# Performance work log

Measured on AMD Instinct MI355X. Metric: run time of the kernel, lower is better.

The kernel has to match this reference:

```python
import jax, jax.numpy as jnp
import numpy as np


def _interpn_linear(vol, loc):
    """Trilinear interpolation matching voxelmorph/neuron interpn.
    vol: [X, Y, Z, C]; loc: [X, Y, Z, 3] absolute sample coordinates.
    """
    spatial = vol.shape[:-1]
    ndims = len(spatial)
    max_f = jnp.asarray([d - 1 for d in spatial], dtype=loc.dtype)
    max_i = jnp.asarray([d - 1 for d in spatial], dtype=jnp.int32)

    loc = jnp.clip(loc, 0.0, max_f)          # clipped_loc
    loc0 = jnp.floor(loc)
    loc0i = jnp.clip(loc0.astype(jnp.int32), 0, max_i)
    loc1i = jnp.clip(loc0i + 1, 0, max_i)

    # voxelmorph weights: corner-0 weight = loc1 - clipped_loc, corner-1 = 1 - that
    w_lo = loc1i.astype(loc.dtype) - loc      # weight for taking loc0
    w_hi = 1.0 - w_lo                          # weight for taking loc1

    out = jnp.zeros(vol.shape, vol.dtype)
    for c in range(2 ** ndims):
        bits = [(c >> d) & 1 for d in range(ndims)]
        idx = tuple(jnp.where(bits[d], loc1i[..., d], loc0i[..., d]) if False else (loc1i[..., d] if bits[d] else loc0i[..., d]) for d in range(ndims))
        w = jnp.ones(loc.shape[:-1], loc.dtype)
        for d in range(ndims):
            w = w * (w_hi[..., d] if bits[d] else w_lo[..., d])
        out = out + vol[idx] * w[..., None]
    return out


def setup_inputs() -> dict:
    key = jax.random.key(0)
    k1, k2 = jax.random.split(key)
    vol = jax.random.normal(k1, (2, 160, 160, 160, 1), dtype=jnp.float32)
    flow = jax.random.normal(k2, (2, 160, 160, 160, 3), dtype=jnp.float32)
    return {"vol": vol, "flow": flow}


def reference(vol, flow):
    # dense displacement field: absolute location = identity grid + flow
    spatial = vol.shape[1:-1]
    grid = jnp.stack(
        jnp.meshgrid(*[jnp.arange(d, dtype=flow.dtype) for d in spatial], indexing="ij"),
        axis=-1,
    )  # [X,Y,Z,3]
    loc = grid[None] + flow  # [B,X,Y,Z,3]
    return jax.vmap(_interpn_linear)(vol, loc)
```

## Files before the change

### kernel.cpp

```cpp
#include <hip/hip_runtime.h>


typedef float f32x4 __attribute__((ext_vector_type(4)));
typedef float f32x2 __attribute__((ext_vector_type(2), aligned(4)));

#define DIM 160
#define DD  (DIM * DIM)
#define DDD (DIM * DIM * DIM)
#define BATCH 2
#define TOTAL (BATCH * DDD)
#define BLK 256
#define NBLK (TOTAL / BLK)
#define NXCD 8
#define CHUNK (NBLK / NXCD)

__global__ __launch_bounds__(256) void st_warp_kernel(
    const float* __restrict__ vol,
    const float* __restrict__ flow,
    float* __restrict__ out)
{
    __shared__ float sflow[BLK * 3];

    int tid = threadIdx.x;
    int bid = blockIdx.x;
    int swz  = (bid & 7) * CHUNK + (bid >> 3);
    int base = swz * BLK;

    const f32x4* fsrc = (const f32x4*)(flow + (size_t)base * 3);
    if (tid < 192) {
        f32x4 v = __builtin_nontemporal_load(&fsrc[tid]);
        ((f32x4*)sflow)[tid] = v;
    }
    __syncthreads();

    int idx = base + tid;

    int b   = idx / DDD;
    int rem = idx - b * DDD;
    int x   = rem / DD;
    int r2  = rem - x * DD;
    int y   = r2 / DIM;
    int z   = r2 - y * DIM;

    float fx = sflow[tid * 3 + 0];
    float fy = sflow[tid * 3 + 1];
    float fz = sflow[tid * 3 + 2];

    const float maxf = (float)(DIM - 1);

    float lx = fminf(fmaxf((float)x + fx, 0.0f), maxf);
    float ly = fminf(fmaxf((float)y + fy, 0.0f), maxf);
    float lz = fminf(fmaxf((float)z + fz, 0.0f), maxf);

    int x0 = (int)floorf(lx);
    int y0 = (int)floorf(ly);
    int z0 = (int)floorf(lz);
    x0 = min(max(x0, 0), DIM - 1);
    y0 = min(max(y0, 0), DIM - 1);
    z0 = min(max(z0, 0), DIM - 1);

    int x1 = min(x0 + 1, DIM - 1);
    int y1 = min(y0 + 1, DIM - 1);
    int z1 = min(z0 + 1, DIM - 1);

    float wx0 = (float)x1 - lx;  float wx1 = 1.0f - wx0;
    float wy0 = (float)y1 - ly;  float wy1 = 1.0f - wy0;
    float wz0 = (float)z1 - lz;  float wz1 = 1.0f - wz0;

    const float* vb = vol + (size_t)b * DDD;

    int bx0 = x0 * DD, bx1 = x1 * DD;
    int by0 = y0 * DIM, by1 = y1 * DIM;

    int zb = min(z0, DIM - 2);
    f32x2 p00 = *(const f32x2*)(vb + bx0 + by0 + zb);
    f32x2 p10 = *(const f32x2*)(vb + bx1 + by0 + zb);
    f32x2 p01 = *(const f32x2*)(vb + bx0 + by1 + zb);
    f32x2 p11 = *(const f32x2*)(vb + bx1 + by1 + zb);

    float v000 = p00.x, v001 = p00.y;
    float v100 = p10.x, v101 = p10.y;
    float v010 = p01.x, v011 = p01.y;
    float v110 = p11.x, v111 = p11.y;

    float acc;
    acc  = v000 * (wx0 * wy0 * wz0);
    acc += v100 * (wx1 * wy0 * wz0);
    acc += v010 * (wx0 * wy1 * wz0);
    acc += v110 * (wx1 * wy1 * wz0);
    acc += v001 * (wx0 * wy0 * wz1);
    acc += v101 * (wx1 * wy0 * wz1);
    acc += v011 * (wx0 * wy1 * wz1);
    acc += v111 * (wx1 * wy1 * wz1);

    __builtin_nontemporal_store(acc, &out[idx]);
}

extern "C" void kernel_launch(void* const* d_in, const int* in_sizes, int n_in,
                              void* d_out, int out_size, void* d_ws, size_t ws_size,
                              hipStream_t stream)
{
    const float* vol  = (const float*)d_in[0];
    const float* flow = (const float*)d_in[1];
    float* out = (float*)d_out;

    st_warp_kernel<<<NBLK, BLK, 0, stream>>>(vol, flow, out);
}
```

Measured before the change: 212.5 us.

## Tile blocks as 4x4x16 bricks for 3D gather locality

Each block now covers a 4x4x16 brick of output voxels instead of 256 contiguous z-voxels (about 1.6 rows). Flow is staged per row into padded shared memory, and the results are transposed through shared memory so the global stores stay contiguous along z. The within-wave thread mapping also changes: each 64-lane wavefront now covers a 4x4x4 cube rather than 64 consecutive z-voxels. The goal is better L2/cache reuse of the trilinear gathers, since neighbouring x/y voxels touch overlapping vol lines. The cost is an extra barrier, shared-memory traffic, and flow loads split into 64-byte row segments that are less coalesced.

```diff
diff --git a/kernel.cpp b/kernel.cpp
--- a/kernel.cpp
+++ b/kernel.cpp
@@ -8,53 +8,68 @@
 #define DD  (DIM * DIM)
 #define DDD (DIM * DIM * DIM)
 #define BATCH 2
-#define TOTAL (BATCH * DDD)
 #define BLK 256
-#define NBLK (TOTAL / BLK)
-#define NXCD 8
-#define CHUNK (NBLK / NXCD)
+#define NBX 40
+#define NBY 40
+#define NBZ 10
+#define NBLK (BATCH * NBX * NBY * NBZ)
+#define CHUNK (NBLK / 8)
+
+#define FROW 52
 
 __global__ __launch_bounds__(256) void st_warp_kernel(
     const float* __restrict__ vol,
     const float* __restrict__ flow,
     float* __restrict__ out)
 {
-    __shared__ float sflow[BLK * 3];
+    __shared__ float sflow[16 * FROW];
+    __shared__ float sout[BLK];
 
     int tid = threadIdx.x;
     int bid = blockIdx.x;
-    int swz  = (bid & 7) * CHUNK + (bid >> 3);
-    int base = swz * BLK;
+    int swz = (bid & 7) * CHUNK + (bid >> 3);
 
-    const f32x4* fsrc = (const f32x4*)(flow + (size_t)base * 3);
+    int bb = swz / (NBX * NBY * NBZ);
+    int r  = swz - bb * (NBX * NBY * NBZ);
+    int xb = r / (NBY * NBZ);
+    int r2 = r - xb * (NBY * NBZ);
+    int yb = r2 / NBZ;
+    int zb = r2 - yb * NBZ;
+
+    int x0b = xb * 4, y0b = yb * 4, z0b = zb * 16;
+
     if (tid < 192) {
-        f32x4 v = __builtin_nontemporal_load(&fsrc[tid]);
-        ((f32x4*)sflow)[tid] = v;
+        int rr = tid / 12;
+        int q  = tid - rr * 12;
+        int xr = x0b + (rr >> 2);
+        int yr = y0b + (rr & 3);
+        const f32x4* src = (const f32x4*)(flow +
+            ((size_t)((bb * DIM + xr) * DIM + yr) * DIM + z0b) * 3);
+        f32x4 v = __builtin_nontemporal_load(&src[q]);
+        *(f32x4*)&sflow[rr * FROW + q * 4] = v;
     }
     __syncthreads();
 
-    int idx = base + tid;
+    int lx  = (tid >> 4) & 3;
+    int ly  = (tid >> 2) & 3;
+    int lz  = ((tid >> 6) << 2) | (tid & 3);
+    int row = (lx << 2) | ly;
 
-    int b   = idx / DDD;
-    int rem = idx - b * DDD;
-    int x   = rem / DD;
-    int r2  = rem - x * DD;
-    int y   = r2 / DIM;
-    int z   = r2 - y * DIM;
+    float fx = sflow[row * FROW + lz * 3 + 0];
+    float fy = sflow[row * FROW + lz * 3 + 1];
+    float fz = sflow[row * FROW + lz * 3 + 2];
 
-    float fx = sflow[tid * 3 + 0];
-    float fy = sflow[tid * 3 + 1];
-    float fz = sflow[tid * 3 + 2];
+    int x = x0b + lx, y = y0b + ly, z = z0b + lz;
 
     const float maxf = (float)(DIM - 1);
 
-    float lx = fminf(fmaxf((float)x + fx, 0.0f), maxf);
-    float ly = fminf(fmaxf((float)y + fy, 0.0f), maxf);
-    float lz = fminf(fmaxf((float)z + fz, 0.0f), maxf);
+    float lxf = fminf(fmaxf((float)x + fx, 0.0f), maxf);
+    float lyf = fminf(fmaxf((float)y + fy, 0.0f), maxf);
+    float lzf = fminf(fmaxf((float)z + fz, 0.0f), maxf);
 
-    int x0 = (int)floorf(lx);
-    int y0 = (int)floorf(ly);
-    int z0 = (int)floorf(lz);
+    int x0 = (int)floorf(lxf);
+    int y0 = (int)floorf(lyf);
+    int z0 = (int)floorf(lzf);
     x0 = min(max(x0, 0), DIM - 1);
     y0 = min(max(y0, 0), DIM - 1);
     z0 = min(max(z0, 0), DIM - 1);
@@ -63,37 +78,41 @@
     int y1 = min(y0 + 1, DIM - 1);
     int z1 = min(z0 + 1, DIM - 1);
 
-    float wx0 = (float)x1 - lx;  float wx1 = 1.0f - wx0;
-    float wy0 = (float)y1 - ly;  float wy1 = 1.0f - wy0;
-    float wz0 = (float)z1 - lz;  float wz1 = 1.0f - wz0;
+    float wx0 = (float)x1 - lxf;  float wx1 = 1.0f - wx0;
+    float wy0 = (float)y1 - lyf;  float wy1 = 1.0f - wy0;
+    float wz0 = (float)z1 - lzf;  float wz1 = 1.0f - wz0;
 
-    const float* vb = vol + (size_t)b * DDD;
-
+    const float* vb = vol + (size_t)bb * DDD;
     int bx0 = x0 * DD, bx1 = x1 * DD;
     int by0 = y0 * DIM, by1 = y1 * DIM;
 
-    int zb = min(z0, DIM - 2);
-    f32x2 p00 = *(const f32x2*)(vb + bx0 + by0 + zb);
-    f32x2 p10 = *(const f32x2*)(vb + bx1 + by0 + zb);
-    f32x2 p01 = *(const f32x2*)(vb + bx0 + by1 + zb);
-    f32x2 p11 = *(const f32x2*)(vb + bx1 + by1 + zb);
-
-    float v000 = p00.x, v001 = p00.y;
-    float v100 = p10.x, v101 = p10.y;
-    float v010 = p01.x, v011 = p01.y;
-    float v110 = p11.x, v111 = p11.y;
+    int zp = min(z0, DIM - 2);
+    f32x2 p00 = *(const f32x2*)(vb + bx0 + by0 + zp);
+    f32x2 p10 = *(const f32x2*)(vb + bx1 + by0 + zp);
+    f32x2 p01 = *(const f32x2*)(vb + bx0 + by1 + zp);
+    f32x2 p11 = *(const f32x2*)(vb + bx1 + by1 + zp);
 
     float acc;
-    acc  = v000 * (wx0 * wy0 * wz0);
-    acc += v100 * (wx1 * wy0 * wz0);
-    acc += v010 * (wx0 * wy1 * wz0);
-    acc += v110 * (wx1 * wy1 * wz0);
-    acc += v001 * (wx0 * wy0 * wz1);
-    acc += v101 * (wx1 * wy0 * wz1);
-    acc += v011 * (wx0 * wy1 * wz1);
-    acc += v111 * (wx1 * wy1 * wz1);
+    acc  = p00.x * (wx0 * wy0 * wz0);
+    acc += p10.x * (wx1 * wy0 * wz0);
+    acc += p01.x * (wx0 * wy1 * wz0);
+    acc += p11.x * (wx1 * wy1 * wz0);
+    acc += p00.y * (wx0 * wy0 * wz1);
+    acc += p10.y * (wx1 * wy0 * wz1);
+    acc += p01.y * (wx0 * wy1 * wz1);
+    acc += p11.y * (wx1 * wy1 * wz1);
 
-    __builtin_nontemporal_store(acc, &out[idx]);
+    sout[tid] = acc;
+    __syncthreads();
+
+    int ro = tid >> 4;
+    int zo = tid & 15;
+    int tsrc = ((zo >> 2) << 6) | ((ro >> 2) << 4) | ((ro & 3) << 2) | (zo & 3);
+    int xs = x0b + (ro >> 2);
+    int ys = y0b + (ro & 3);
+    float v = sout[tsrc];
+    __builtin_nontemporal_store(v,
+        &out[(size_t)((bb * DIM + xs) * DIM + ys) * DIM + z0b + zo]);
 }
 
 extern "C" void kernel_launch(void* const* d_in, const int* in_sizes, int n_in,
```

After: 202.7 us. 1.05x faster.
